# Performance work log

Hardware: AMD Instinct MI355X
Metric: run time of the kernel (lower is better)

## Reference

```python
import jax, jax.numpy as jnp
import numpy as np

B, S, D, H = 4, 2048, 1024, 16
HD = D // H  # head_dim = 64


def setup_inputs() -> dict:
    key = jax.random.key(0)
    k1, k2, k3 = jax.random.split(key, 3)
    scale = 0.02
    return {
        "hidden_states": jax.random.normal(k1, (B, S, D), dtype=jnp.float32),
        "W_attn": jax.random.normal(k2, (D, 3 * D), dtype=jnp.float32) * scale,
        "b_attn": jnp.zeros((3 * D,), dtype=jnp.float32),
        "W_proj": jax.random.normal(k3, (D, D), dtype=jnp.float32) * scale,
        "b_proj": jnp.zeros((D,), dtype=jnp.float32),
    }


def reference(hidden_states, W_attn, b_attn, W_proj, b_proj):
    b, s, d = hidden_states.shape
    qkv = hidden_states @ W_attn + b_attn  # [B,S,3D]
    q, k, v = jnp.split(qkv, 3, axis=-1)
    # [B,S,D] -> [B,H,S,hd]
    def to_heads(x):
        return x.reshape(b, s, H, HD).transpose(0, 2, 1, 3)
    q, k, v = to_heads(q), to_heads(k), to_heads(v)
    scores = jnp.einsum("bhqd,bhkd->bhqk", q, k) / jnp.sqrt(jnp.float32(HD))
    causal = jnp.tril(jnp.ones((s, s), dtype=bool))  # [S,S]
    scores = jnp.where(causal[None, None], scores, jnp.float32(-jnp.inf))
    probs = jax.nn.softmax(scores, axis=-1)  # dropout p=0 -> identity (eval)
    out = jnp.einsum("bhqk,bhkd->bhqd", probs, v)  # [B,H,S,hd]
    out = out.transpose(0, 2, 1, 3).reshape(b, s, d)
    return out @ W_proj + b_proj
```

## Files before the change

### kernel.cpp

```cpp
#include <hip/hip_runtime.h>
#include <hip/hip_bf16.h>


typedef float f32x4 __attribute__((ext_vector_type(4)));
typedef __bf16 bf16x8 __attribute__((ext_vector_type(8)));
typedef unsigned short u16x8 __attribute__((ext_vector_type(8)));
typedef unsigned short u16x4 __attribute__((ext_vector_type(4)));

static constexpr int Sq = 2048, Dm = 1024, HD = 64, N3 = 3072;
static constexpr int Mrows = 4 * Sq;
static constexpr float SM_SCALE = 0.18033688011112042f;
static constexpr float SM_BIAS  = -11.541560327111707f;

__device__ __forceinline__ float bf2f(unsigned short u) {
  union { unsigned u32; float f; } x; x.u32 = ((unsigned)u) << 16; return x.f;
}
__device__ __forceinline__ unsigned short f2bf(float f) {
  return __builtin_bit_cast(unsigned short, (__bf16)f);
}
__device__ __forceinline__ f32x4 mfma16(u16x8 a, u16x8 b, f32x4 c) {
  return __builtin_amdgcn_mfma_f32_16x16x32_bf16(
      __builtin_bit_cast(bf16x8, a), __builtin_bit_cast(bf16x8, b), c, 0, 0, 0);
}

__global__ __launch_bounds__(256) void cvt_k(
    const float* __restrict__ in, unsigned short* __restrict__ out, int n) {
  int stride = gridDim.x * 256 * 4;
  for (int i = (blockIdx.x * 256 + threadIdx.x) * 4; i < n; i += stride) {
    f32x4 v = *reinterpret_cast<const f32x4*>(&in[i]);
    u16x4 o;
    #pragma unroll
    for (int j = 0; j < 4; j++) o[j] = f2bf(v[j]);
    *reinterpret_cast<u16x4*>(&out[i]) = o;
  }
}

__global__ __launch_bounds__(256) void tcvt_k(
    const float* __restrict__ in, unsigned short* __restrict__ out,
    int R, int C) {
  __shared__ float tile[32][33];
  int c0 = blockIdx.x * 32, r0 = blockIdx.y * 32;
  int tx = threadIdx.x & 31, ty = threadIdx.x >> 5;
  #pragma unroll
  for (int i = 0; i < 32; i += 8)
    tile[ty + i][tx] = in[(size_t)(r0 + ty + i) * C + c0 + tx];
  __syncthreads();
  #pragma unroll
  for (int i = 0; i < 32; i += 8)
    out[(size_t)(c0 + ty + i) * R + r0 + tx] = f2bf(tile[tx][ty + i]);
}

template <bool OUT_F32>
__global__ __launch_bounds__(256) void gemm_bt(
    const unsigned short* __restrict__ A, const unsigned short* __restrict__ Bt,
    const float* __restrict__ bias, void* __restrict__ Cout,
    int Md, int Nd, int Kd) {
  __shared__ unsigned short Asm[128 * 32];
  __shared__ unsigned short Bsm[128 * 32];
  int t = threadIdx.x;
  int wave = t >> 6, lane = t & 63;
  int lrow = lane & 15, lq = lane >> 4;
  int wr = wave >> 1, wc = wave & 1;
  int bm = blockIdx.y * 128, bn = blockIdx.x * 128;
  f32x4 acc[4][4] = {};

  for (int k0 = 0; k0 < Kd; k0 += 32) {
    __syncthreads();
    #pragma unroll
    for (int c = 0; c < 2; c++) {
      int e = c * 2048 + t * 8;
      int row = e >> 5, col = e & 31;
      const unsigned short* ga = A + (size_t)(bm + row) * Kd + k0 + col;
      const unsigned short* gb = Bt + (size_t)(bn + row) * Kd + k0 + col;
      __builtin_amdgcn_global_load_lds(
          (const __attribute__((address_space(1))) void*)ga,
          (__attribute__((address_space(3))) void*)((char*)Asm + c * 4096 + wave * 1024),
          16, 0, 0);
      __builtin_amdgcn_global_load_lds(
          (const __attribute__((address_space(1))) void*)gb,
          (__attribute__((address_space(3))) void*)((char*)Bsm + c * 4096 + wave * 1024),
          16, 0, 0);
    }
    __syncthreads();

    u16x8 af[4], bfr[4];
    #pragma unroll
    for (int m = 0; m < 4; m++)
      af[m] = *reinterpret_cast<const u16x8*>(&Asm[(wr * 64 + m * 16 + lrow) * 32 + lq * 8]);
    #pragma unroll
    for (int n = 0; n < 4; n++)
      bfr[n] = *reinterpret_cast<const u16x8*>(&Bsm[(wc * 64 + n * 16 + lrow) * 32 + lq * 8]);
    #pragma unroll
    for (int m = 0; m < 4; m++)
      #pragma unroll
      for (int n = 0; n < 4; n++)
        acc[m][n] = mfma16(af[m], bfr[n], acc[m][n]);
  }

  #pragma unroll
  for (int n = 0; n < 4; n++) {
    int col = bn + wc * 64 + n * 16 + lrow;
    float bv = bias[col];
    #pragma unroll
    for (int m = 0; m < 4; m++) {
      #pragma unroll
      for (int j = 0; j < 4; j++) {
        int row = bm + wr * 64 + m * 16 + lq * 4 + j;
        if constexpr (OUT_F32)
          ((float*)Cout)[(size_t)row * Nd + col] = acc[m][n][j] + bv;
        else
          ((unsigned short*)Cout)[(size_t)row * Nd + col] = f2bf(acc[m][n][j] + bv);
      }
    }
  }
}

__global__ __launch_bounds__(256) void attn_k(
    const unsigned short* __restrict__ qkv,
    unsigned short* __restrict__ ao) {
  int bh = blockIdx.y;
  int b = bh >> 4, h = bh & 15;
  int t = threadIdx.x, wave = t >> 6, lane = t & 63;
  int lrow = lane & 15, lq = lane >> 4;

  __shared__ unsigned short Kl[2][64][72];
  __shared__ unsigned short Vt[2][64][72];
  __shared__ unsigned short Pl[4][16][72];

  const size_t base = (size_t)b * Sq * N3;
  const unsigned short* Kbase = qkv + base + Dm + h * HD;
  const unsigned short* Vbase = qkv + base + 2 * Dm + h * HD;

  int irow = t >> 2, icol = (t & 3) * 16;
  int vd = lane, vkb = wave;

  u16x8 ones;
  #pragma unroll
  for (int j = 0; j < 8; j++) ones[j] = 0x3F80;

  u16x8 kr0, kr1, vr0, vr1;
  auto prefetch = [&](int kv) {
    const unsigned short* kp = Kbase + (size_t)(kv + irow) * N3 + icol;
    kr0 = *reinterpret_cast<const u16x8*>(kp);
    kr1 = *reinterpret_cast<const u16x8*>(kp + 8);
    const unsigned short* vp = Vbase + (size_t)kv * N3 + vd;
    #pragma unroll
    for (int i = 0; i < 8; i++) {
      vr0[i] = vp[(size_t)(vkb * 8 + i) * N3];
      vr1[i] = vp[(size_t)(32 + vkb * 8 + i) * N3];
    }
  };

  int bsel = 0;

  #pragma unroll 1
  for (int pass = 0; pass < 2; ++pass) {
    int qb = pass ? (int)blockIdx.x : 31 - (int)blockIdx.x;
    int q0 = qb * 64;
    int ntiles = qb + 1;
    int rwm = q0 + wave * 16;

    u16x8 qf0, qf1;
    {
      const unsigned short* qp =
          qkv + base + (size_t)(rwm + lrow) * N3 + h * HD + lq * 8;
      u16x8 r0 = *reinterpret_cast<const u16x8*>(qp);
      u16x8 r1 = *reinterpret_cast<const u16x8*>(qp + 32);
      #pragma unroll
      for (int j = 0; j < 8; j++) {
        qf0[j] = f2bf(SM_SCALE * bf2f(r0[j]));
        qf1[j] = f2bf(SM_SCALE * bf2f(r1[j]));
      }
    }

    f32x4 oacc[4] = {};
    f32x4 dacc = {};

    if (pass == 0) prefetch(0);

    #pragma unroll 1
    for (int kt = 0; kt < ntiles; ++kt) {
      int kv = kt * 64;
      *reinterpret_cast<u16x8*>(&Kl[bsel][irow][icol]) = kr0;
      *reinterpret_cast<u16x8*>(&Kl[bsel][irow][icol + 8]) = kr1;
      *reinterpret_cast<u16x8*>(&Vt[bsel][vd][vkb * 8]) = vr0;
      *reinterpret_cast<u16x8*>(&Vt[bsel][vd][32 + vkb * 8]) = vr1;
      if (kt + 1 < ntiles) prefetch(kv + 64);
      else if (pass == 0) prefetch(0);
      __syncthreads();

      f32x4 sacc[4];
      #pragma unroll
      for (int ct = 0; ct < 4; ct++)
        sacc[ct] = f32x4{SM_BIAS, SM_BIAS, SM_BIAS, SM_BIAS};
      #pragma unroll
      for (int ct = 0; ct < 4; ct++) {
        u16x8 kf0 = *reinterpret_cast<const u16x8*>(&Kl[bsel][ct * 16 + lrow][lq * 8]);
        u16x8 kf1 = *reinterpret_cast<const u16x8*>(&Kl[bsel][ct * 16 + lrow][32 + lq * 8]);
        sacc[ct] = mfma16(kf0, qf0, sacc[ct]);
        sacc[ct] = mfma16(kf1, qf1, sacc[ct]);
      }

      bool need_mask = kv + 63 > rwm;
      int dlim = rwm - kv + lrow;
      #pragma unroll
      for (int ct = 0; ct < 4; ct++) {
        u16x4 o;
        #pragma unroll
        for (int j = 0; j < 4; j++) {
          float e = exp2f(sacc[ct][j]);
          if (need_mask) e = (16 * ct + 4 * lq + j <= dlim) ? e : 0.f;
          o[j] = f2bf(e);
        }
        *reinterpret_cast<u16x4*>(&Pl[wave][lrow][16 * ct + 4 * lq]) = o;
      }

      u16x8 pa0 = *reinterpret_cast<const u16x8*>(&Pl[wave][lrow][lq * 8]);
      u16x8 pa1 = *reinterpret_cast<const u16x8*>(&Pl[wave][lrow][32 + lq * 8]);
      dacc = mfma16(pa0, ones, dacc);
      dacc = mfma16(pa1, ones, dacc);
      #pragma unroll
      for (int ht = 0; ht < 4; ht++) {
        u16x8 vf0 = *reinterpret_cast<const u16x8*>(&Vt[bsel][ht * 16 + lrow][lq * 8]);
        u16x8 vf1 = *reinterpret_cast<const u16x8*>(&Vt[bsel][ht * 16 + lrow][32 + lq * 8]);
        oacc[ht] = mfma16(pa0, vf0, oacc[ht]);
        oacc[ht] = mfma16(pa1, vf1, oacc[ht]);
      }
      bsel ^= 1;
    }

    float inv[4];
    #pragma unroll
    for (int j = 0; j < 4; j++) inv[j] = __builtin_amdgcn_rcpf(dacc[j]);
    #pragma unroll
    for (int ht = 0; ht < 4; ht++)
      #pragma unroll
      for (int j = 0; j < 4; j++) {
        int rg = rwm + lq * 4 + j;
        float v = oacc[ht][j] * inv[j];
        ao[(size_t)(b * Sq + rg) * Dm + h * HD + ht * 16 + lrow] = f2bf(v);
      }
  }
}

extern "C" void kernel_launch(void* const* d_in, const int* in_sizes, int n_in,
                              void* d_out, int out_size, void* d_ws, size_t ws_size,
                              hipStream_t stream) {
  const float* hs = (const float*)d_in[0];
  const float* Wa = (const float*)d_in[1];
  const float* ba = (const float*)d_in[2];
  const float* Wp = (const float*)d_in[3];
  const float* bp = (const float*)d_in[4];
  float* out = (float*)d_out;

  char* ws = (char*)d_ws;
  unsigned short* QKV = (unsigned short*)ws;
  unsigned short* WaT = (unsigned short*)(ws + 50331648);
  unsigned short* AO  = (unsigned short*)(ws + 50331648);
  unsigned short* WpT = (unsigned short*)ws;
  unsigned short* hsB = (unsigned short*)d_out;

  cvt_k<<<2048, 256, 0, stream>>>(hs, hsB, Mrows * Dm);
  tcvt_k<<<dim3(96, 32), 256, 0, stream>>>(Wa, WaT, 1024, 3072);
  gemm_bt<false><<<dim3(24, 64), 256, 0, stream>>>(hsB, WaT, ba, QKV, Mrows, N3, Dm);
  attn_k<<<dim3(16, 64), 256, 0, stream>>>(QKV, AO);
  tcvt_k<<<dim3(32, 32), 256, 0, stream>>>(Wp, WpT, 1024, 1024);
  gemm_bt<true><<<dim3(8, 64), 256, 0, stream>>>(AO, WpT, bp, out, Mrows, Dm, Dm);
}
```

Measured before the change: 228.7 us.

## Widen attention blocks to 128 query rows with split K/V staging waves

The attention kernel now runs 512-thread blocks covering 128 query rows, with half the grid along the query axis, so each staged K/V tile serves eight waves instead of four. Waves 0-3 load K and waves 4-7 load the transposed V, which cuts per-thread staging work and halves global K/V reads per query row. It also hoists the K-fragment LDS reads ahead of the QK MFMAs and raises wave priority with s_setprio around the MFMA sections. The tradeoff is fewer blocks, with possible occupancy or register pressure under launch_bounds(512,4) and more fully masked work for the lower waves on diagonal tiles.

```diff
diff --git a/kernel.cpp b/kernel.cpp
--- a/kernel.cpp
+++ b/kernel.cpp
@@ -115,7 +115,7 @@
   }
 }
 
-__global__ __launch_bounds__(256) void attn_k(
+__global__ __launch_bounds__(512, 4) void attn_k(
     const unsigned short* __restrict__ qkv,
     unsigned short* __restrict__ ao) {
   int bh = blockIdx.y;
@@ -125,51 +125,53 @@
 
   __shared__ unsigned short Kl[2][64][72];
   __shared__ unsigned short Vt[2][64][72];
-  __shared__ unsigned short Pl[4][16][72];
+  __shared__ unsigned short Pl[8][16][72];
 
   const size_t base = (size_t)b * Sq * N3;
   const unsigned short* Kbase = qkv + base + Dm + h * HD;
   const unsigned short* Vbase = qkv + base + 2 * Dm + h * HD;
 
+  bool stageK = wave < 4;
   int irow = t >> 2, icol = (t & 3) * 16;
-  int vd = lane, vkb = wave;
+  int vd = t & 63, vkb = (t >> 6) & 3;
 
   u16x8 ones;
   #pragma unroll
   for (int j = 0; j < 8; j++) ones[j] = 0x3F80;
 
-  u16x8 kr0, kr1, vr0, vr1;
+  u16x8 r0, r1;
   auto prefetch = [&](int kv) {
-    const unsigned short* kp = Kbase + (size_t)(kv + irow) * N3 + icol;
-    kr0 = *reinterpret_cast<const u16x8*>(kp);
-    kr1 = *reinterpret_cast<const u16x8*>(kp + 8);
-    const unsigned short* vp = Vbase + (size_t)kv * N3 + vd;
-    #pragma unroll
-    for (int i = 0; i < 8; i++) {
-      vr0[i] = vp[(size_t)(vkb * 8 + i) * N3];
-      vr1[i] = vp[(size_t)(32 + vkb * 8 + i) * N3];
+    if (stageK) {
+      const unsigned short* kp = Kbase + (size_t)(kv + irow) * N3 + icol;
+      r0 = *reinterpret_cast<const u16x8*>(kp);
+      r1 = *reinterpret_cast<const u16x8*>(kp + 8);
+    } else {
+      const unsigned short* vp = Vbase + (size_t)kv * N3 + vd;
+      #pragma unroll
+      for (int i = 0; i < 8; i++) {
+        r0[i] = vp[(size_t)(vkb * 8 + i) * N3];
+        r1[i] = vp[(size_t)(32 + vkb * 8 + i) * N3];
+      }
     }
   };
-
-  int bsel = 0;
 
   #pragma unroll 1
   for (int pass = 0; pass < 2; ++pass) {
-    int qb = pass ? (int)blockIdx.x : 31 - (int)blockIdx.x;
-    int q0 = qb * 64;
-    int ntiles = qb + 1;
+    int qb = pass ? (int)blockIdx.x : 15 - (int)blockIdx.x;
+    int q0 = qb * 128;
+    int ntiles = 2 * qb + 2;
     int rwm = q0 + wave * 16;
 
     u16x8 qf0, qf1;
     {
       const unsigned short* qp =
           qkv + base + (size_t)(rwm + lrow) * N3 + h * HD + lq * 8;
-      u16x8 r0 = *reinterpret_cast<const u16x8*>(qp);
-      u16x8 r1 = *reinterpret_cast<const u16x8*>(qp + 32);
+      u16x8 a0 = *reinterpret_cast<const u16x8*>(qp);
+      u16x8 a1 = *reinterpret_cast<const u16x8*>(qp + 32);
       #pragma unroll
       for (int j = 0; j < 8; j++) {
-        qf0[j] = f2bf(SM_SCALE * bf2f(r0[j]));
-        qf1[j] = f2bf(SM_SCALE * bf2f(r1[j]));
+        qf0[j] = f2bf(SM_SCALE * bf2f(a0[j]));
+        qf1[j] = f2bf(SM_SCALE * bf2f(a1[j]));
       }
     }
 
@@ -180,26 +182,35 @@
 
     #pragma unroll 1
     for (int kt = 0; kt < ntiles; ++kt) {
-      int kv = kt * 64;
-      *reinterpret_cast<u16x8*>(&Kl[bsel][irow][icol]) = kr0;
-      *reinterpret_cast<u16x8*>(&Kl[bsel][irow][icol + 8]) = kr1;
-      *reinterpret_cast<u16x8*>(&Vt[bsel][vd][vkb * 8]) = vr0;
-      *reinterpret_cast<u16x8*>(&Vt[bsel][vd][32 + vkb * 8]) = vr1;
+      int kv = kt * 64, bsel = kt & 1;
+      if (stageK) {
+        *reinterpret_cast<u16x8*>(&Kl[bsel][irow][icol]) = r0;
+        *reinterpret_cast<u16x8*>(&Kl[bsel][irow][icol + 8]) = r1;
+      } else {
+        *reinterpret_cast<u16x8*>(&Vt[bsel][vd][vkb * 8]) = r0;
+        *reinterpret_cast<u16x8*>(&Vt[bsel][vd][32 + vkb * 8]) = r1;
+      }
       if (kt + 1 < ntiles) prefetch(kv + 64);
       else if (pass == 0) prefetch(0);
       __syncthreads();
 
+      u16x8 kf0[4], kf1[4];
+      #pragma unroll
+      for (int ct = 0; ct < 4; ct++) {
+        kf0[ct] = *reinterpret_cast<const u16x8*>(&Kl[bsel][ct * 16 + lrow][lq * 8]);
+        kf1[ct] = *reinterpret_cast<const u16x8*>(&Kl[bsel][ct * 16 + lrow][32 + lq * 8]);
+      }
       f32x4 sacc[4];
       #pragma unroll
       for (int ct = 0; ct < 4; ct++)
         sacc[ct] = f32x4{SM_BIAS, SM_BIAS, SM_BIAS, SM_BIAS};
+      __builtin_amdgcn_s_setprio(1);
       #pragma unroll
       for (int ct = 0; ct < 4; ct++) {
-        u16x8 kf0 = *reinterpret_cast<const u16x8*>(&Kl[bsel][ct * 16 + lrow][lq * 8]);
-        u16x8 kf1 = *reinterpret_cast<const u16x8*>(&Kl[bsel][ct * 16 + lrow][32 + lq * 8]);
-        sacc[ct] = mfma16(kf0, qf0, sacc[ct]);
-        sacc[ct] = mfma16(kf1, qf1, sacc[ct]);
-      }
+        sacc[ct] = mfma16(kf0[ct], qf0, sacc[ct]);
+        sacc[ct] = mfma16(kf1[ct], qf1, sacc[ct]);
+      }
+      __builtin_amdgcn_s_setprio(0);
 
       bool need_mask = kv + 63 > rwm;
       int dlim = rwm - kv + lrow;
@@ -217,6 +228,7 @@
 
       u16x8 pa0 = *reinterpret_cast<const u16x8*>(&Pl[wave][lrow][lq * 8]);
       u16x8 pa1 = *reinterpret_cast<const u16x8*>(&Pl[wave][lrow][32 + lq * 8]);
+      __builtin_amdgcn_s_setprio(1);
       dacc = mfma16(pa0, ones, dacc);
       dacc = mfma16(pa1, ones, dacc);
       #pragma unroll
@@ -226,7 +238,7 @@
         oacc[ht] = mfma16(pa0, vf0, oacc[ht]);
         oacc[ht] = mfma16(pa1, vf1, oacc[ht]);
       }
-      bsel ^= 1;
+      __builtin_amdgcn_s_setprio(0);
     }
 
     float inv[4];
@@ -263,7 +275,7 @@
   cvt_k<<<2048, 256, 0, stream>>>(hs, hsB, Mrows * Dm);
   tcvt_k<<<dim3(96, 32), 256, 0, stream>>>(Wa, WaT, 1024, 3072);
   gemm_bt<false><<<dim3(24, 64), 256, 0, stream>>>(hsB, WaT, ba, QKV, Mrows, N3, Dm);
-  attn_k<<<dim3(16, 64), 256, 0, stream>>>(QKV, AO);
+  attn_k<<<dim3(8, 64), 512, 0, stream>>>(QKV, AO);
   tcvt_k<<<dim3(32, 32), 256, 0, stream>>>(Wp, WpT, 1024, 1024);
   gemm_bt<true><<<dim3(8, 64), 256, 0, stream>>>(AO, WpT, bp, out, Mrows, Dm, Dm);
 }
```

Measured after the change: 208.0 us. 9.0% less time.
